# Kernel tuning notes

Measured on AMD Instinct MI355X. Metric: run time of the kernel, lower is better.

## Reference

```python
import jax, jax.numpy as jnp
import numpy as np

N, F_NODE, F_FLOW, H, E, B, L = 131072, 64, 16, 128, 2097152, 256, 32


def setup_inputs() -> dict:
    key = jax.random.key(0)
    ks = jax.random.split(key, 24)
    gn = lambda k, s, sc: jax.random.normal(k, s, jnp.float32) * sc
    s_in = 1.0 / np.sqrt(F_NODE)
    s_h = 1.0 / np.sqrt(H)
    s_f = 1.0 / np.sqrt(F_FLOW)
    s_c = 1.0 / np.sqrt(2 * H + H // 2)
    inp = {
        "x": gn(ks[0], (N, F_NODE), 1.0),
        "edge_index": jax.random.randint(ks[1], (2, E), 0, N),
        "batch": jnp.sort(jax.random.randint(ks[2], (N,), 0, B)),
        "path_idx": jax.random.randint(ks[3], (B, L), 0, N),
        "path_len": jax.random.randint(ks[4], (B,), 1, L + 1),
        "flow": gn(ks[5], (B, F_FLOW), 1.0),
        # SAGEConv1: out = mean_agg(x_j) @ Wl.T + b + x_i @ Wr.T
        "Wl1": gn(ks[6], (H, F_NODE), s_in), "Wr1": gn(ks[7], (H, F_NODE), s_in), "b1": gn(ks[8], (H,), s_in),
        "Wl2": gn(ks[9], (H, H), s_h), "Wr2": gn(ks[10], (H, H), s_h), "b2": gn(ks[11], (H,), s_h),
        # LSTM (torch gate order i,f,g,o)
        "Wih": gn(ks[12], (4 * H, H), s_h), "Whh": gn(ks[13], (4 * H, H), s_h),
        "bih": gn(ks[14], (4 * H,), s_h), "bhh": gn(ks[15], (4 * H,), s_h),
        # flow encoder Linear(F_FLOW, H//2)
        "Wf": gn(ks[16], (H // 2, F_FLOW), s_f), "bf": gn(ks[17], (H // 2,), s_f),
        # scorer MLP: Linear(2H+H//2, H) -> ReLU -> Linear(H, 1)
        "Ws1": gn(ks[18], (H, 2 * H + H // 2), s_c), "bs1": gn(ks[19], (H,), s_c),
        "Ws2": gn(ks[20], (1, H), s_h), "bs2": gn(ks[21], (1,), s_h),
    }
    return inp


def _sage(x, src, dst, Wl, Wr, b, n):
    agg = jax.ops.segment_sum(x[src], dst, num_segments=n)  # [n, d]
    cnt = jax.ops.segment_sum(jnp.ones((src.shape[0],), x.dtype), dst, num_segments=n)
    mean = agg / jnp.maximum(cnt, 1.0)[:, None]
    return mean @ Wl.T + b + x @ Wr.T


def _lstm_final_h(seq, valid, Wih, Whh, bih, bhh):
    # seq: [B, L, H], valid: [B, L] bool; returns h at each path's last valid step
    b, l, h = seq.shape
    h0 = jnp.zeros((b, h), seq.dtype)

    def step(carry, inp):
        hp, cp = carry
        x_t, v = inp  # [B,H], [B]
        gates = x_t @ Wih.T + hp @ Whh.T + bih + bhh
        i, f, g, o = jnp.split(gates, 4, axis=-1)
        c_new = jax.nn.sigmoid(f) * cp + jax.nn.sigmoid(i) * jnp.tanh(g)
        h_new = jax.nn.sigmoid(o) * jnp.tanh(c_new)
        m = v[:, None]
        return (jnp.where(m, h_new, hp), jnp.where(m, c_new, cp)), None

    (hf, _), _ = jax.lax.scan(step, (h0, h0),
                              (jnp.swapaxes(seq, 0, 1), jnp.swapaxes(valid, 0, 1)))
    return hf


def reference(x, edge_index, batch, path_idx, path_len, flow,
              Wl1, Wr1, b1, Wl2, Wr2, b2,
              Wih, Whh, bih, bhh, Wf, bf, Ws1, bs1, Ws2, bs2):
    n = x.shape[0]
    src, dst = edge_index[0], edge_index[1]
    h1 = jax.nn.relu(_sage(x, src, dst, Wl1, Wr1, b1, n))
    node_emb = jax.nn.relu(_sage(h1, src, dst, Wl2, Wr2, b2, n))

    # global mean pool per graph
    gsum = jax.ops.segment_sum(node_emb, batch, num_segments=B)
    gcnt = jax.ops.segment_sum(jnp.ones((n,), node_emb.dtype), batch, num_segments=B)
    graph_emb = gsum / jnp.maximum(gcnt, 1.0)[:, None]  # [B, H]

    flow_emb = jax.nn.relu(flow @ Wf.T + bf)  # [B, H//2]

    path_seq = node_emb[path_idx]  # [B, L, H]
    valid = jnp.arange(L)[None, :] < path_len[:, None]  # [B, L]
    path_emb = _lstm_final_h(path_seq, valid, Wih, Whh, bih, bhh)  # [B, H]

    combined = jnp.concatenate([graph_emb, path_emb, flow_emb], axis=-1)
    hidden = jax.nn.relu(combined @ Ws1.T + bs1)
    scores = hidden @ Ws2.T + bs2  # [B, 1]
    return scores[:, 0]  # matches torch.cat of per-path [1] outputs -> [B]
```

## Files before the change

### kernel.cpp

```cpp
#include <hip/hip_runtime.h>
#include <hip/hip_bf16.h>

#define N_NODES 131072
#define N_EDGES 2097152
#define BATCHES 256
#define LPATH   32
#define NB   256
#define NPB  512
#define GB   256
#define EPB  8192
#define EBL_CAP 9216

typedef __hip_bfloat16 bf16;
using short8  = __attribute__((ext_vector_type(8))) short;
using floatx4 = __attribute__((ext_vector_type(4))) float;
using floatx2 = __attribute__((ext_vector_type(2))) float;

__device__ __forceinline__ float bl(unsigned u){ union {unsigned x; float f;} c; c.x = u << 16; return c.f; }
__device__ __forceinline__ float bh(unsigned u){ union {unsigned x; float f;} c; c.x = u & 0xffff0000u; return c.f; }
__device__ __forceinline__ unsigned packbf(float lo, float hi){
  bf16 l = __float2bfloat16(lo), h = __float2bfloat16(hi);
  unsigned short lu, hu;
  __builtin_memcpy(&lu, &l, 2); __builtin_memcpy(&hu, &h, 2);
  return (unsigned)lu | ((unsigned)hu << 16);
}
__device__ __forceinline__ float frcp(float x){ return __builtin_amdgcn_rcpf(x); }
__device__ __forceinline__ float sigf(float x){ return frcp(1.f + __expf(-x)); }
__device__ __forceinline__ float tanh_fast(float x){ return fmaf(2.f, frcp(1.f + __expf(-2.f * x)), -1.f); }

__global__ void mega0_k(const float* __restrict__ x, unsigned* __restrict__ xb8, bf16* __restrict__ Acat1,
                        const int* __restrict__ dst, int* __restrict__ cntA,
                        const float* __restrict__ Wl1, const float* __restrict__ Wr1,
                        const float* __restrict__ Wl2, const float* __restrict__ Wr2,
                        const float* __restrict__ Wih, const float* __restrict__ Whh,
                        const float* __restrict__ bih, const float* __restrict__ bhh,
                        bf16* __restrict__ Wcat1, bf16* __restrict__ Wcat2,
                        bf16* __restrict__ WihB, bf16* __restrict__ WhhB, float* __restrict__ bsumF,
                        const int* __restrict__ batch, int* __restrict__ starts){
  __shared__ int h[NB];
  int bid = blockIdx.x, tid = threadIdx.x;
  if (bid < 8192){
    int g = bid * 256 + tid;
    int n = g >> 4, p = g & 15;
    float4 v = *(const float4*)(x + (size_t)n * 64 + p * 4);
    uint2 wb; wb.x = packbf(v.x, v.y); wb.y = packbf(v.z, v.w);
    *(uint2*)(Acat1 + (size_t)n * 128 + 64 + p * 4) = wb;
    int w = 0;
    w = __builtin_amdgcn_cvt_pk_fp8_f32(v.x, v.y, w, false);
    w = __builtin_amdgcn_cvt_pk_fp8_f32(v.z, v.w, w, true);
    xb8[(size_t)n * 16 + p] = (unsigned)w;
  } else if (bid < 8448){
    int cb = bid - 8192;
    h[tid] = 0;
    __syncthreads();
    int base = cb * EPB;
    #pragma unroll
    for (int i = 0; i < EPB / 256; ++i){
      int d = dst[base + i * 256 + tid];
      atomicAdd(&h[d >> 9], 1);
    }
    __syncthreads();
    cntA[tid * GB + cb] = h[tid];
  } else if (bid < 9155){
    int g = (bid - 8448) * 256 + tid;
    if (g < 16384) {
      int hh = g >> 7, k = g & 127;
      float v = (k < 64) ? Wl1[hh * 64 + k] : Wr1[hh * 64 + (k - 64)];
      Wcat1[g] = __float2bfloat16(v);
    } else if (g < 49152) {
      int q = g - 16384;
      int hh = q >> 8, k = q & 255;
      float v = (k < 128) ? Wl2[hh * 128 + k] : Wr2[hh * 128 + (k - 128)];
      Wcat2[q] = __float2bfloat16(v);
    } else if (g < 114688) {
      int q = g - 49152;
      WihB[q] = __float2bfloat16(Wih[q]);
    } else if (g < 180224) {
      int q = g - 114688;
      WhhB[q] = __float2bfloat16(Whh[q]);
    } else if (g < 180736) {
      int k = g - 180224;
      bsumF[k] = bih[k] + bhh[k];
    }
  } else {
    int b = tid;
    int lo = 0, hi = N_NODES;
    while (lo < hi){ int mid = (lo + hi) >> 1; if (batch[mid] < b) lo = mid + 1; else hi = mid; }
    starts[b] = lo;
    if (b == 0) starts[BATCHES] = N_NODES;
  }
}

__global__ void scan1_k(const int* __restrict__ cnt, int* __restrict__ ofsA, int* __restrict__ bsum){
  __shared__ int sh[256];
  int t = threadIdx.x, i = blockIdx.x * 256 + t;
  int v = cnt[i];
  sh[t] = v; __syncthreads();
  int inc = v;
  for (int d = 1; d < 256; d <<= 1){
    int add = (t >= d) ? sh[t - d] : 0;
    __syncthreads();
    inc += add; sh[t] = inc;
    __syncthreads();
  }
  ofsA[i] = inc - v;
  if (t == 255) bsum[blockIdx.x] = inc;
}

__global__ void passA2_k(const int* __restrict__ src, const int* __restrict__ dst,
                         const int* __restrict__ ofsA, const int* __restrict__ bsum,
                         unsigned* __restrict__ ebuf){
  __shared__ int cur[NB];
  __shared__ int sc[NB];
  int tid = threadIdx.x;
  int v = bsum[tid];
  sc[tid] = v; __syncthreads();
  int inc = v;
  for (int d = 1; d < NB; d <<= 1){
    int add = (tid >= d) ? sc[tid - d] : 0;
    __syncthreads();
    inc += add; sc[tid] = inc;
    __syncthreads();
  }
  cur[tid] = ofsA[tid * GB + blockIdx.x] + (inc - v);
  __syncthreads();
  int base = blockIdx.x * EPB;
  #pragma unroll
  for (int i = 0; i < EPB / 256; ++i){
    int e = base + i * 256 + tid;
    int s = src[e], d = dst[e];
    int p = atomicAdd(&cur[d >> 9], 1);
    ebuf[p] = (unsigned)s | ((unsigned)(d & (NPB - 1)) << 17);
  }
}

__global__ void passB_k(const unsigned* __restrict__ ebuf, const int* __restrict__ bsum,
                        int* __restrict__ offs, int* __restrict__ srcS){
  __shared__ unsigned ebl[EBL_CAP];
  __shared__ int ncnt[NPB];
  __shared__ int pairs[256];
  __shared__ int nofs[NPB];
  __shared__ int sc[NB];
  int k = blockIdx.x, tid = threadIdx.x;
  int v = bsum[tid];
  sc[tid] = v; __syncthreads();
  int inc0 = v;
  for (int d = 1; d < NB; d <<= 1){
    int add = (tid >= d) ? sc[tid - d] : 0;
    __syncthreads();
    inc0 += add; sc[tid] = inc0;
    __syncthreads();
  }
  sc[tid] = inc0 - v;
  __syncthreads();
  int bs = sc[k];
  int be = (k < NB - 1) ? sc[k + 1] : N_EDGES;
  int cnt = be - bs;
  int stg = cnt < EBL_CAP ? cnt : EBL_CAP;
  for (int i = tid; i < stg; i += 256) ebl[i] = ebuf[bs + i];
  ncnt[tid] = 0; ncnt[tid + 256] = 0;
  __syncthreads();
  for (int i = tid; i < cnt; i += 256){
    unsigned w = (i < stg) ? ebl[i] : ebuf[bs + i];
    atomicAdd(&ncnt[w >> 17], 1);
  }
  __syncthreads();
  int p = ncnt[2 * tid] + ncnt[2 * tid + 1];
  pairs[tid] = p;
  __syncthreads();
  int inc = p;
  for (int d = 1; d < 256; d <<= 1){
    int add = (tid >= d) ? pairs[tid - d] : 0;
    __syncthreads();
    inc += add; pairs[tid] = inc;
    __syncthreads();
  }
  int ex = inc - p;
  nofs[2 * tid]     = ex;
  nofs[2 * tid + 1] = ex + ncnt[2 * tid];
  __syncthreads();
  offs[k * NPB + tid]       = bs + nofs[tid];
  offs[k * NPB + tid + 256] = bs + nofs[tid + 256];
  if (k == NB - 1 && tid == 0) offs[N_NODES] = N_EDGES;
  ncnt[tid] = nofs[tid]; ncnt[tid + 256] = nofs[tid + 256];
  __syncthreads();
  for (int i = tid; i < cnt; i += 256){
    unsigned w = (i < stg) ? ebl[i] : ebuf[bs + i];
    int loc = w >> 17, sv = w & 0x1FFFF;
    int pp = atomicAdd(&ncnt[loc], 1);
    srcS[bs + pp] = sv;
  }
}

__global__ void agg1_k(const unsigned* __restrict__ xb8, const int* __restrict__ offs,
                       const int* __restrict__ srcS, bf16* __restrict__ Acat1){
  int wid = threadIdx.x >> 6, lane = threadIdx.x & 63;
  int q = lane >> 4;
  int slot = (lane >> 3) & 1, fl = lane & 7;
  int n = blockIdx.x * 16 + wid * 4 + q;
  int s = offs[n], e = offs[n + 1];
  floatx2 a0={0,0}, a1={0,0}, a2={0,0}, a3={0,0};
  floatx2 c0={0,0}, c1={0,0}, c2={0,0}, c3={0,0};
  int i = s + slot;
  for (; i + 6 < e; i += 8){
    int sv0 = srcS[i], sv1 = srcS[i + 2], sv2 = srcS[i + 4], sv3 = srcS[i + 6];
    uint2 u = *(const uint2*)(xb8 + (size_t)sv0 * 16 + fl * 2);
    uint2 v = *(const uint2*)(xb8 + (size_t)sv1 * 16 + fl * 2);
    uint2 w = *(const uint2*)(xb8 + (size_t)sv2 * 16 + fl * 2);
    uint2 z = *(const uint2*)(xb8 + (size_t)sv3 * 16 + fl * 2);
    a0 += __builtin_amdgcn_cvt_pk_f32_fp8(u.x, false);
    a1 += __builtin_amdgcn_cvt_pk_f32_fp8(u.x, true);
    a2 += __builtin_amdgcn_cvt_pk_f32_fp8(u.y, false);
    a3 += __builtin_amdgcn_cvt_pk_f32_fp8(u.y, true);
    c0 += __builtin_amdgcn_cvt_pk_f32_fp8(v.x, false);
    c1 += __builtin_amdgcn_cvt_pk_f32_fp8(v.x, true);
    c2 += __builtin_amdgcn_cvt_pk_f32_fp8(v.y, false);
    c3 += __builtin_amdgcn_cvt_pk_f32_fp8(v.y, true);
    a0 += __builtin_amdgcn_cvt_pk_f32_fp8(w.x, false);
    a1 += __builtin_amdgcn_cvt_pk_f32_fp8(w.x, true);
    a2 += __builtin_amdgcn_cvt_pk_f32_fp8(w.y, false);
    a3 += __builtin_amdgcn_cvt_pk_f32_fp8(w.y, true);
    c0 += __builtin_amdgcn_cvt_pk_f32_fp8(z.x, false);
    c1 += __builtin_amdgcn_cvt_pk_f32_fp8(z.x, true);
    c2 += __builtin_amdgcn_cvt_pk_f32_fp8(z.y, false);
    c3 += __builtin_amdgcn_cvt_pk_f32_fp8(z.y, true);
  }
  for (; i < e; i += 2){
    int sv0 = srcS[i];
    uint2 u = *(const uint2*)(xb8 + (size_t)sv0 * 16 + fl * 2);
    a0 += __builtin_amdgcn_cvt_pk_f32_fp8(u.x, false);
    a1 += __builtin_amdgcn_cvt_pk_f32_fp8(u.x, true);
    a2 += __builtin_amdgcn_cvt_pk_f32_fp8(u.y, false);
    a3 += __builtin_amdgcn_cvt_pk_f32_fp8(u.y, true);
  }
  a0 += c0; a1 += c1; a2 += c2; a3 += c3;
  float f[8] = {a0.x, a0.y, a1.x, a1.y, a2.x, a2.y, a3.x, a3.y};
  #pragma unroll
  for (int j = 0; j < 8; ++j)
    f[j] += __shfl_xor(f[j], 8);
  if (slot == 0){
    int d = e - s; if (d < 1) d = 1;
    float inv = 1.f / (float)d;
    uint4 w;
    w.x = packbf(f[0] * inv, f[1] * inv);
    w.y = packbf(f[2] * inv, f[3] * inv);
    w.z = packbf(f[4] * inv, f[5] * inv);
    w.w = packbf(f[6] * inv, f[7] * inv);
    *(uint4*)(Acat1 + (size_t)n * 128 + fl * 8) = w;
  }
}

__global__ __launch_bounds__(256) void gemmf8_k(const bf16* __restrict__ A, const bf16* __restrict__ W,
                                                const float* __restrict__ bias,
                                                bf16* __restrict__ h1B, unsigned* __restrict__ h1f8){
  __shared__ bf16 Wl[128][136];
  __shared__ unsigned char f8t[64][144];
  int tid = threadIdx.x;
  int wid = tid >> 6, lane = tid & 63;
  int l16 = lane & 15, quad = lane >> 4;
  int rowBase = blockIdx.x * 64 + wid * 16;
  floatx4 acc[8] = {};
  for (int c = tid; c < 2048; c += 256){
    int r = c >> 4, kc = (c & 15) << 3;
    *(uint4*)(&Wl[r][kc]) = *(const uint4*)(W + (size_t)r * 128 + kc);
  }
  __syncthreads();
  for (int kk = 0; kk < 4; ++kk){
    short8 af = *(const short8*)(A + (size_t)(rowBase + l16) * 128 + kk * 32 + quad * 8);
    #pragma unroll
    for (int c = 0; c < 8; ++c){
      short8 bq = *(const short8*)(&Wl[c * 16 + l16][kk * 32 + quad * 8]);
      acc[c] = __builtin_amdgcn_mfma_f32_16x16x32_bf16(af, bq, acc[c], 0, 0, 0);
    }
  }
  #pragma unroll
  for (int c = 0; c < 8; ++c){
    int col = c * 16 + l16;
    float bv = bias[col];
    #pragma unroll
    for (int r = 0; r < 4; ++r){
      int rl = wid * 16 + quad * 4 + r;
      float v = fmaxf(acc[c][r] + bv, 0.f);
      h1B[(size_t)(blockIdx.x * 64 + rl) * 128 + col] = __float2bfloat16(v);
      unsigned pk = (unsigned)__builtin_amdgcn_cvt_pk_fp8_f32(v, v, 0, false);
      f8t[rl][col] = (unsigned char)(pk & 0xFF);
    }
  }
  __syncthreads();
  for (int it = tid; it < 512; it += 256){
    int row = it >> 3, seg = it & 7;
    uint4 val = *(const uint4*)(&f8t[row][seg * 16]);
    *(uint4*)((char*)h1f8 + (size_t)(blockIdx.x * 64 + row) * 128 + seg * 16) = val;
  }
}

__global__ void agg2_k(const int* __restrict__ offs, const int* __restrict__ srcS,
                       const unsigned* __restrict__ h1f8, bf16* __restrict__ meanB){
  int wid = threadIdx.x >> 6, lane = threadIdx.x & 63;
  int half = lane >> 5;
  int slot = (lane >> 4) & 1, fl = lane & 15;
  int n = blockIdx.x * 8 + wid * 2 + half;
  int s = offs[n], e = offs[n + 1];
  floatx2 a0={0,0}, a1={0,0}, a2={0,0}, a3={0,0};
  floatx2 c0={0,0}, c1={0,0}, c2={0,0}, c3={0,0};
  int i = s + slot;
  for (; i + 6 < e; i += 8){
    int sv0 = srcS[i], sv1 = srcS[i + 2], sv2 = srcS[i + 4], sv3 = srcS[i + 6];
    uint2 u = *(const uint2*)(h1f8 + (size_t)sv0 * 32 + fl * 2);
    uint2 v = *(const uint2*)(h1f8 + (size_t)sv1 * 32 + fl * 2);
    uint2 w = *(const uint2*)(h1f8 + (size_t)sv2 * 32 + fl * 2);
    uint2 z = *(const uint2*)(h1f8 + (size_t)sv3 * 32 + fl * 2);
    a0 += __builtin_amdgcn_cvt_pk_f32_fp8(u.x, false);
    a1 += __builtin_amdgcn_cvt_pk_f32_fp8(u.x, true);
    a2 += __builtin_amdgcn_cvt_pk_f32_fp8(u.y, false);
    a3 += __builtin_amdgcn_cvt_pk_f32_fp8(u.y, true);
    c0 += __builtin_amdgcn_cvt_pk_f32_fp8(v.x, false);
    c1 += __builtin_amdgcn_cvt_pk_f32_fp8(v.x, true);
    c2 += __builtin_amdgcn_cvt_pk_f32_fp8(v.y, false);
    c3 += __builtin_amdgcn_cvt_pk_f32_fp8(v.y, true);
    a0 += __builtin_amdgcn_cvt_pk_f32_fp8(w.x, false);
    a1 += __builtin_amdgcn_cvt_pk_f32_fp8(w.x, true);
    a2 += __builtin_amdgcn_cvt_pk_f32_fp8(w.y, false);
    a3 += __builtin_amdgcn_cvt_pk_f32_fp8(w.y, true);
    c0 += __builtin_amdgcn_cvt_pk_f32_fp8(z.x, false);
    c1 += __builtin_amdgcn_cvt_pk_f32_fp8(z.x, true);
    c2 += __builtin_amdgcn_cvt_pk_f32_fp8(z.y, false);
    c3 += __builtin_amdgcn_cvt_pk_f32_fp8(z.y, true);
  }
  for (; i < e; i += 2){
    int sv0 = srcS[i];
    uint2 u = *(const uint2*)(h1f8 + (size_t)sv0 * 32 + fl * 2);
    a0 += __builtin_amdgcn_cvt_pk_f32_fp8(u.x, false);
    a1 += __builtin_amdgcn_cvt_pk_f32_fp8(u.x, true);
    a2 += __builtin_amdgcn_cvt_pk_f32_fp8(u.y, false);
    a3 += __builtin_amdgcn_cvt_pk_f32_fp8(u.y, true);
  }
  a0 += c0; a1 += c1; a2 += c2; a3 += c3;
  float f[8] = {a0.x, a0.y, a1.x, a1.y, a2.x, a2.y, a3.x, a3.y};
  #pragma unroll
  for (int j = 0; j < 8; ++j)
    f[j] += __shfl_xor(f[j], 16);
  if (slot == 0){
    int d = e - s; if (d < 1) d = 1;
    float inv = 1.f / (float)d;
    uint4 w;
    w.x = packbf(f[0] * inv, f[1] * inv);
    w.y = packbf(f[2] * inv, f[3] * inv);
    w.z = packbf(f[4] * inv, f[5] * inv);
    w.w = packbf(f[6] * inv, f[7] * inv);
    *(uint4*)(meanB + (size_t)n * 128 + fl * 8) = w;
  }
}

__global__ __launch_bounds__(256) void gemm2sp_k(const bf16* __restrict__ A0, const bf16* __restrict__ A1,
                                                 const bf16* __restrict__ W, const float* __restrict__ bias,
                                                 bf16* __restrict__ out){
  __shared__ bf16 Wl[128][136];
  int tid = threadIdx.x;
  int wid = tid >> 6, lane = tid & 63;
  int l16 = lane & 15, quad = lane >> 4;
  int rowBase = blockIdx.x * 64 + wid * 16;
  floatx4 acc[8] = {};
  #pragma unroll
  for (int ks = 0; ks < 2; ++ks){
    __syncthreads();
    for (int c = tid; c < 2048; c += 256){
      int r = c >> 4, kc = (c & 15) << 3;
      *(uint4*)(&Wl[r][kc]) = *(const uint4*)(W + (size_t)r * 256 + ks * 128 + kc);
    }
    __syncthreads();
    const bf16* Ab = ks ? A1 : A0;
    for (int kk = 0; kk < 4; ++kk){
      short8 af = *(const short8*)(Ab + (size_t)(rowBase + l16) * 128 + kk * 32 + quad * 8);
      #pragma unroll
      for (int c = 0; c < 8; ++c){
        short8 bq = *(const short8*)(&Wl[c * 16 + l16][kk * 32 + quad * 8]);
        acc[c] = __builtin_amdgcn_mfma_f32_16x16x32_bf16(af, bq, acc[c], 0, 0, 0);
      }
    }
  }
  #pragma unroll
  for (int c = 0; c < 8; ++c){
    int col = c * 16 + l16;
    float bv = bias[col];
    #pragma unroll
    for (int r = 0; r < 4; ++r){
      int row = rowBase + quad * 4 + r;
      out[(size_t)row * 128 + col] = __float2bfloat16(fmaxf(acc[c][r] + bv, 0.f));
    }
  }
}

__global__ __launch_bounds__(256) void tail0_k(const bf16* __restrict__ ne, const bf16* __restrict__ W,
                                               const float* __restrict__ bias, float* __restrict__ pre,
                                               const int* __restrict__ ridx,
                                               const int* __restrict__ starts,
                                               const float* __restrict__ flow, const float* __restrict__ Wf,
                                               const float* __restrict__ bfv, float* __restrict__ comb){
  __shared__ bf16 Wl[128][136];
  __shared__ float sh[4][128];
  int bid = blockIdx.x, tid = threadIdx.x;
  if (bid < 512){
    int bx = bid >> 2, by = bid & 3;
    int wid = tid >> 6, lane = tid & 63;
    int l16 = lane & 15, quad = lane >> 4;
    int rowBase = bx * 64 + wid * 16;
    int colGroup = by * 128;
    int arow = ridx[rowBase + l16];
    floatx4 acc[8] = {};
    for (int c = tid; c < 2048; c += 256){
      int r = c >> 4, kc = (c & 15) << 3;
      *(uint4*)(&Wl[r][kc]) = *(const uint4*)(W + (size_t)(colGroup + r) * 128 + kc);
    }
    __syncthreads();
    for (int kk = 0; kk < 4; ++kk){
      short8 af = *(const short8*)(ne + (size_t)arow * 128 + kk * 32 + quad * 8);
      #pragma unroll
      for (int c = 0; c < 8; ++c){
        short8 bq = *(const short8*)(&Wl[c * 16 + l16][kk * 32 + quad * 8]);
        acc[c] = __builtin_amdgcn_mfma_f32_16x16x32_bf16(af, bq, acc[c], 0, 0, 0);
      }
    }
    #pragma unroll
    for (int c = 0; c < 8; ++c){
      int col = colGroup + c * 16 + l16;
      float bv = bias[col];
      #pragma unroll
      for (int r = 0; r < 4; ++r){
        int row = rowBase + quad * 4 + r;
        pre[(size_t)row * 512 + col] = acc[c][r] + bv;
      }
    }
  } else if (bid < 768){
    int b = bid - 512;
    int q = tid >> 6, lane = tid & 63;
    int s = starts[b], e = starts[b + 1];
    float a0 = 0.f, a1 = 0.f;
    for (int i = s + q; i < e; i += 4){
      unsigned u = *(const unsigned*)(ne + (size_t)i * 128 + lane * 2);
      a0 += bl(u); a1 += bh(u);
    }
    sh[q][lane * 2] = a0; sh[q][lane * 2 + 1] = a1;
    __syncthreads();
    if (tid < 128){
      int f = tid;
      float tot = sh[0][f] + sh[1][f] + sh[2][f] + sh[3][f];
      int d = e - s; if (d < 1) d = 1;
      comb[b * 320 + f] = tot / (float)d;
    }
  } else {
    int g = (bid - 768) * 256 + tid;
    int b = g >> 6, j = g & 63;
    float acc = bfv[j];
    for (int k = 0; k < 16; ++k)
      acc += flow[b * 16 + k] * Wf[j * 16 + k];
    comb[b * 320 + 256 + j] = fmaxf(acc, 0.f);
  }
}

__global__ __launch_bounds__(256, 1) void lstm_k(const bf16* __restrict__ Whh, const float* __restrict__ pre,
                                                 const int* __restrict__ path_len, float* __restrict__ comb){
  __shared__ bf16 hbuf[2][16][136];
  int tid = threadIdx.x;
  int w = tid >> 6, lane = tid & 63;
  int l16 = lane & 15, quad = lane >> 4;
  int b0 = blockIdx.x * 16;

  short8 wb[4][2][4];
  #pragma unroll
  for (int q = 0; q < 4; ++q)
    #pragma unroll
    for (int hf = 0; hf < 2; ++hf){
      const bf16* rp = Whh + (size_t)(q * 128 + w * 32 + hf * 16 + l16) * 128 + quad * 8;
      #pragma unroll
      for (int ks = 0; ks < 4; ++ks) wb[q][hf][ks] = *(const short8*)(rp + ks * 32);
    }

  int lenr[4];
  #pragma unroll
  for (int r = 0; r < 4; ++r){
    int L = path_len[b0 + quad * 4 + r];
    if (L < 1) L = 1; if (L > LPATH) L = LPATH;
    lenr[r] = L;
  }
  int maxlen = 1;
  for (int i = 0; i < 16; ++i){
    int L = path_len[b0 + i];
    if (L > LPATH) L = LPATH;
    if (L > maxlen) maxlen = L;
  }

  for (int i = tid; i < 1088; i += 256) ((unsigned*)&hbuf[0][0][0])[i] = 0;

  const float* pb[4];
  #pragma unroll
  for (int r = 0; r < 4; ++r)
    pb[r] = pre + (size_t)(b0 + quad * 4 + r) * LPATH * 512 + w * 32 + l16;

  float pv[4][2][4];
  #pragma unroll
  for (int q = 0; q < 4; ++q)
    #pragma unroll
    for (int hf = 0; hf < 2; ++hf)
      #pragma unroll
      for (int r = 0; r < 4; ++r)
        pv[q][hf][r] = pb[r][q * 128 + hf * 16];

  float cst[2][4] = {}, hst[2][4] = {};

  for (int t = 0; t < maxlen; ++t){
    int cur = t & 1, nxt = cur ^ 1;
    __syncthreads();
    short8 af[4];
    #pragma unroll
    for (int ks = 0; ks < 4; ++ks)
      af[ks] = *(const short8*)(&hbuf[cur][l16][ks * 32 + quad * 8]);
    int tn = (t + 1 < maxlen) ? t + 1 : t;
    float pnext[4][2][4];
    #pragma unroll
    for (int q = 0; q < 4; ++q)
      #pragma unroll
      for (int hf = 0; hf < 2; ++hf)
        #pragma unroll
        for (int r = 0; r < 4; ++r)
          pnext[q][hf][r] = pb[r][tn * 512 + q * 128 + hf * 16];
    floatx4 acc[4][2];
    #pragma unroll
    for (int q = 0; q < 4; ++q)
      #pragma unroll
      for (int hf = 0; hf < 2; ++hf){
        acc[q][hf][0] = pv[q][hf][0]; acc[q][hf][1] = pv[q][hf][1];
        acc[q][hf][2] = pv[q][hf][2]; acc[q][hf][3] = pv[q][hf][3];
      }
    #pragma unroll
    for (int ks = 0; ks < 4; ++ks)
      #pragma unroll
      for (int q = 0; q < 4; ++q)
        #pragma unroll
        for (int hf = 0; hf < 2; ++hf)
          acc[q][hf] = __builtin_amdgcn_mfma_f32_16x16x32_bf16(af[ks], wb[q][hf][ks], acc[q][hf], 0, 0, 0);
    #pragma unroll
    for (int hf = 0; hf < 2; ++hf)
      #pragma unroll
      for (int r = 0; r < 4; ++r){
        float ig = sigf(acc[0][hf][r]);
        float fg = sigf(acc[1][hf][r]);
        float gg = tanh_fast(acc[2][hf][r]);
        float og = sigf(acc[3][hf][r]);
        float cn = fmaf(fg, cst[hf][r], ig * gg);
        float hn = og * tanh_fast(cn);
        bool vld = t < lenr[r];
        cst[hf][r] = vld ? cn : cst[hf][r];
        hst[hf][r] = vld ? hn : hst[hf][r];
        hbuf[nxt][quad * 4 + r][w * 32 + hf * 16 + l16] = __float2bfloat16(hst[hf][r]);
      }
    #pragma unroll
    for (int q = 0; q < 4; ++q)
      #pragma unroll
      for (int hf = 0; hf < 2; ++hf)
        #pragma unroll
        for (int r = 0; r < 4; ++r)
          pv[q][hf][r] = pnext[q][hf][r];
  }

  #pragma unroll
  for (int hf = 0; hf < 2; ++hf)
    #pragma unroll
    for (int r = 0; r < 4; ++r)
      comb[(b0 + quad * 4 + r) * 320 + 128 + w * 32 + hf * 16 + l16] = hst[hf][r];
}

__global__ void head_k(const float* __restrict__ comb, const float* __restrict__ Ws1, const float* __restrict__ bs1,
                       const float* __restrict__ Ws2, const float* __restrict__ bs2, float* __restrict__ out){
  __shared__ float cl[320];
  __shared__ float red[128];
  int b = blockIdx.x, j = threadIdx.x;
  for (int k = j; k < 320; k += 128) cl[k] = comb[b * 320 + k];
  __syncthreads();
  float acc = bs1[j];
  const float4* wr = (const float4*)(Ws1 + (size_t)j * 320);
  #pragma unroll 4
  for (int kc = 0; kc < 80; ++kc){
    float4 u = wr[kc];
    int k = kc * 4;
    acc += u.x * cl[k] + u.y * cl[k + 1] + u.z * cl[k + 2] + u.w * cl[k + 3];
  }
  float hv = fmaxf(acc, 0.f);
  red[j] = hv * Ws2[j];
  __syncthreads();
  for (int s = 64; s > 0; s >>= 1){ if (j < s) red[j] += red[j + s]; __syncthreads(); }
  if (j == 0) out[b] = red[0] + bs2[0];
}

constexpr size_t OFF_OFFS   = 0;
constexpr size_t OFF_CNTA   = 524544;
constexpr size_t OFF_OFSA   = OFF_CNTA   + 262144;
constexpr size_t OFF_BSUM   = OFF_OFSA   + 262144;
constexpr size_t OFF_STARTS = OFF_BSUM   + 1024;
constexpr size_t OFF_SRCS   = OFF_STARTS + 2048;
constexpr size_t OFF_WCAT1  = OFF_SRCS   + 8388608;
constexpr size_t OFF_WCAT2  = OFF_WCAT1  + 32768;
constexpr size_t OFF_WIHB   = OFF_WCAT2  + 65536;
constexpr size_t OFF_WHHB   = OFF_WIHB   + 131072;
constexpr size_t OFF_BSUMF  = OFF_WHHB   + 131072;
constexpr size_t OFF_COMB   = OFF_BSUMF  + 2048;
constexpr size_t OFF_R1     = OFF_COMB   + 327680;
constexpr size_t OFF_R2     = OFF_R1     + 33554432;
constexpr size_t OFF_EBUF   = OFF_R2;
constexpr size_t OFF_H1B    = OFF_R2;
constexpr size_t OFF_PRE    = OFF_R2;
constexpr size_t OFF_XB8    = OFF_R2 + 33554432;
constexpr size_t OFF_H1F8   = OFF_R2 + 33554432;
constexpr size_t OFF_NE     = OFF_R2 + 33554432;

extern "C" void kernel_launch(void* const* d_in, const int* in_sizes, int n_in,
                              void* d_out, int out_size, void* d_ws, size_t ws_size,
                              hipStream_t stream){
  const float* x      = (const float*)d_in[0];
  const int* edge     = (const int*)d_in[1];
  const int* batch    = (const int*)d_in[2];
  const int* path_idx = (const int*)d_in[3];
  const int* path_len = (const int*)d_in[4];
  const float* flow   = (const float*)d_in[5];
  const float* Wl1 = (const float*)d_in[6];
  const float* Wr1 = (const float*)d_in[7];
  const float* b1  = (const float*)d_in[8];
  const float* Wl2 = (const float*)d_in[9];
  const float* Wr2 = (const float*)d_in[10];
  const float* b2  = (const float*)d_in[11];
  const float* Wih = (const float*)d_in[12];
  const float* Whh = (const float*)d_in[13];
  const float* bih = (const float*)d_in[14];
  const float* bhh = (const float*)d_in[15];
  const float* Wf  = (const float*)d_in[16];
  const float* bfv = (const float*)d_in[17];
  const float* Ws1 = (const float*)d_in[18];
  const float* bs1 = (const float*)d_in[19];
  const float* Ws2 = (const float*)d_in[20];
  const float* bs2 = (const float*)d_in[21];

  char* ws = (char*)d_ws;
  int* offs    = (int*)(ws + OFF_OFFS);
  int* cntA    = (int*)(ws + OFF_CNTA);
  int* ofsA    = (int*)(ws + OFF_OFSA);
  int* bsum    = (int*)(ws + OFF_BSUM);
  int* starts  = (int*)(ws + OFF_STARTS);
  int* srcS    = (int*)(ws + OFF_SRCS);
  bf16* Wcat1  = (bf16*)(ws + OFF_WCAT1);
  bf16* Wcat2  = (bf16*)(ws + OFF_WCAT2);
  bf16* WihB   = (bf16*)(ws + OFF_WIHB);
  bf16* WhhB   = (bf16*)(ws + OFF_WHHB);
  float* bsumF = (float*)(ws + OFF_BSUMF);
  float* comb  = (float*)(ws + OFF_COMB);
  bf16* Acat1  = (bf16*)(ws + OFF_R1);
  bf16* meanB  = (bf16*)(ws + OFF_R1);
  unsigned* ebuf = (unsigned*)(ws + OFF_EBUF);
  bf16* h1B    = (bf16*)(ws + OFF_H1B);
  float* pre   = (float*)(ws + OFF_PRE);
  unsigned* xb8  = (unsigned*)(ws + OFF_XB8);
  unsigned* h1f8 = (unsigned*)(ws + OFF_H1F8);
  bf16* node_emb = (bf16*)(ws + OFF_NE);

  mega0_k<<<9156, 256, 0, stream>>>(x, xb8, Acat1, edge + N_EDGES, cntA,
                                    Wl1, Wr1, Wl2, Wr2, Wih, Whh, bih, bhh,
                                    Wcat1, Wcat2, WihB, WhhB, bsumF, batch, starts);
  scan1_k<<<NB, 256, 0, stream>>>(cntA, ofsA, bsum);
  passA2_k<<<GB, 256, 0, stream>>>(edge, edge + N_EDGES, ofsA, bsum, ebuf);
  passB_k<<<NB, 256, 0, stream>>>(ebuf, bsum, offs, srcS);
  agg1_k<<<N_NODES / 16, 256, 0, stream>>>(xb8, offs, srcS, Acat1);
  gemmf8_k<<<N_NODES / 64, 256, 0, stream>>>(Acat1, Wcat1, b1, h1B, h1f8);
  agg2_k<<<N_NODES / 8, 256, 0, stream>>>(offs, srcS, h1f8, meanB);
  gemm2sp_k<<<N_NODES / 64, 256, 0, stream>>>(meanB, h1B, Wcat2, b2, node_emb);
  tail0_k<<<832, 256, 0, stream>>>(node_emb, WihB, bsumF, pre, path_idx, starts, flow, Wf, bfv, comb);
  lstm_k<<<BATCHES / 16, 256, 0, stream>>>(WhhB, pre, path_len, comb);
  head_k<<<BATCHES, 128, 0, stream>>>(comb, Ws1, bs1, Ws2, bs2, (float*)d_out);
}
```

Baseline: 389.1 us.

## Fuse graph mean-pool into GEMM epilogue and drop separate scan kernel

Removes the scan1 kernel by having passA2 and passB each recompute per-bucket totals and prefixes directly from the count matrix. Also moves the global mean-pool sum into the second SAGE GEMM epilogue: each block segment-reduces its rows by batch id in shared memory and atomically adds into comb, with the divide by node count deferred to the head kernel. The aim is fewer launches and no second read of node_emb, at the cost of redundant 256-element row sums per thread, more shared memory in the GEMM, and float atomics whose order is nondeterministic.

```diff
diff --git a/kernel.cpp b/kernel.cpp
--- a/kernel.cpp
+++ b/kernel.cpp
@@ -36,7 +36,7 @@
                         const float* __restrict__ bih, const float* __restrict__ bhh,
                         bf16* __restrict__ Wcat1, bf16* __restrict__ Wcat2,
                         bf16* __restrict__ WihB, bf16* __restrict__ WhhB, float* __restrict__ bsumF,
-                        const int* __restrict__ batch, int* __restrict__ starts){
+                        const int* __restrict__ batch, int* __restrict__ starts, float* __restrict__ comb){
   __shared__ int h[NB];
   int bid = blockIdx.x, tid = threadIdx.x;
   if (bid < 8192){
@@ -82,49 +82,42 @@
       int k = g - 180224;
       bsumF[k] = bih[k] + bhh[k];
     }
-  } else {
+  } else if (bid == 9155){
     int b = tid;
     int lo = 0, hi = N_NODES;
     while (lo < hi){ int mid = (lo + hi) >> 1; if (batch[mid] < b) lo = mid + 1; else hi = mid; }
     starts[b] = lo;
     if (b == 0) starts[BATCHES] = N_NODES;
-  }
-}
-
-__global__ void scan1_k(const int* __restrict__ cnt, int* __restrict__ ofsA, int* __restrict__ bsum){
-  __shared__ int sh[256];
-  int t = threadIdx.x, i = blockIdx.x * 256 + t;
-  int v = cnt[i];
-  sh[t] = v; __syncthreads();
-  int inc = v;
-  for (int d = 1; d < 256; d <<= 1){
-    int add = (t >= d) ? sh[t - d] : 0;
-    __syncthreads();
-    inc += add; sh[t] = inc;
-    __syncthreads();
-  }
-  ofsA[i] = inc - v;
-  if (t == 255) bsum[blockIdx.x] = inc;
+  } else {
+    int g = (bid - 9156) * 256 + tid;
+    int b = g >> 7, f = g & 127;
+    comb[b * 320 + f] = 0.f;
+  }
 }
 
 __global__ void passA2_k(const int* __restrict__ src, const int* __restrict__ dst,
-                         const int* __restrict__ ofsA, const int* __restrict__ bsum,
-                         unsigned* __restrict__ ebuf){
+                         const int* __restrict__ cntA, unsigned* __restrict__ ebuf){
   __shared__ int cur[NB];
   __shared__ int sc[NB];
-  int tid = threadIdx.x;
-  int v = bsum[tid];
-  sc[tid] = v; __syncthreads();
-  int inc = v;
+  int tid = threadIdx.x, bid = blockIdx.x;
+  const int* row = cntA + tid * GB;
+  int pref = 0, tot = 0;
+  for (int j = 0; j < GB; ++j){
+    int c = row[j];
+    tot += c;
+    if (j < bid) pref += c;
+  }
+  sc[tid] = tot; __syncthreads();
+  int inc = tot;
   for (int d = 1; d < NB; d <<= 1){
     int add = (tid >= d) ? sc[tid - d] : 0;
     __syncthreads();
     inc += add; sc[tid] = inc;
     __syncthreads();
   }
-  cur[tid] = ofsA[tid * GB + blockIdx.x] + (inc - v);
-  __syncthreads();
-  int base = blockIdx.x * EPB;
+  cur[tid] = (inc - tot) + pref;
+  __syncthreads();
+  int base = bid * EPB;
   #pragma unroll
   for (int i = 0; i < EPB / 256; ++i){
     int e = base + i * 256 + tid;
@@ -134,7 +127,7 @@
   }
 }
 
-__global__ void passB_k(const unsigned* __restrict__ ebuf, const int* __restrict__ bsum,
+__global__ void passB_k(const unsigned* __restrict__ ebuf, const int* __restrict__ cntA,
                         int* __restrict__ offs, int* __restrict__ srcS){
   __shared__ unsigned ebl[EBL_CAP];
   __shared__ int ncnt[NPB];
@@ -142,16 +135,18 @@
   __shared__ int nofs[NPB];
   __shared__ int sc[NB];
   int k = blockIdx.x, tid = threadIdx.x;
-  int v = bsum[tid];
-  sc[tid] = v; __syncthreads();
-  int inc0 = v;
+  const int* row = cntA + tid * GB;
+  int tot = 0;
+  for (int j = 0; j < GB; ++j) tot += row[j];
+  sc[tid] = tot; __syncthreads();
+  int inc0 = tot;
   for (int d = 1; d < NB; d <<= 1){
     int add = (tid >= d) ? sc[tid - d] : 0;
     __syncthreads();
     inc0 += add; sc[tid] = inc0;
     __syncthreads();
   }
-  sc[tid] = inc0 - v;
+  sc[tid] = inc0 - tot;
   __syncthreads();
   int bs = sc[k];
   int be = (k < NB - 1) ? sc[k + 1] : N_EDGES;
@@ -354,8 +349,11 @@
 
 __global__ __launch_bounds__(256) void gemm2sp_k(const bf16* __restrict__ A0, const bf16* __restrict__ A1,
                                                  const bf16* __restrict__ W, const float* __restrict__ bias,
-                                                 bf16* __restrict__ out){
+                                                 bf16* __restrict__ out,
+                                                 const int* __restrict__ batch, float* __restrict__ comb){
   __shared__ bf16 Wl[128][136];
+  __shared__ float vals[64][132];
+  __shared__ int bid64[64];
   int tid = threadIdx.x;
   int wid = tid >> 6, lane = tid & 63;
   int l16 = lane & 15, quad = lane >> 4;
@@ -379,26 +377,39 @@
       }
     }
   }
+  if (tid < 64) bid64[tid] = batch[blockIdx.x * 64 + tid];
   #pragma unroll
   for (int c = 0; c < 8; ++c){
     int col = c * 16 + l16;
     float bv = bias[col];
     #pragma unroll
     for (int r = 0; r < 4; ++r){
-      int row = rowBase + quad * 4 + r;
-      out[(size_t)row * 128 + col] = __float2bfloat16(fmaxf(acc[c][r] + bv, 0.f));
-    }
-  }
+      int rl = wid * 16 + quad * 4 + r;
+      float v = fmaxf(acc[c][r] + bv, 0.f);
+      out[(size_t)(blockIdx.x * 64 + rl) * 128 + col] = __float2bfloat16(v);
+      vals[rl][col] = v;
+    }
+  }
+  __syncthreads();
+  int col = tid & 127, hf = tid >> 7;
+  int r0 = hf * 32;
+  int curb = bid64[r0];
+  float run = 0.f;
+  #pragma unroll 8
+  for (int r = r0; r < r0 + 32; ++r){
+    int bb = bid64[r];
+    if (bb != curb){ atomicAdd(&comb[curb * 320 + col], run); run = 0.f; curb = bb; }
+    run += vals[r][col];
+  }
+  atomicAdd(&comb[curb * 320 + col], run);
 }
 
 __global__ __launch_bounds__(256) void tail0_k(const bf16* __restrict__ ne, const bf16* __restrict__ W,
                                                const float* __restrict__ bias, float* __restrict__ pre,
                                                const int* __restrict__ ridx,
-                                               const int* __restrict__ starts,
                                                const float* __restrict__ flow, const float* __restrict__ Wf,
                                                const float* __restrict__ bfv, float* __restrict__ comb){
   __shared__ bf16 Wl[128][136];
-  __shared__ float sh[4][128];
   int bid = blockIdx.x, tid = threadIdx.x;
   if (bid < 512){
     int bx = bid >> 2, by = bid & 3;
@@ -431,25 +442,8 @@
         pre[(size_t)row * 512 + col] = acc[c][r] + bv;
       }
     }
-  } else if (bid < 768){
-    int b = bid - 512;
-    int q = tid >> 6, lane = tid & 63;
-    int s = starts[b], e = starts[b + 1];
-    float a0 = 0.f, a1 = 0.f;
-    for (int i = s + q; i < e; i += 4){
-      unsigned u = *(const unsigned*)(ne + (size_t)i * 128 + lane * 2);
-      a0 += bl(u); a1 += bh(u);
-    }
-    sh[q][lane * 2] = a0; sh[q][lane * 2 + 1] = a1;
-    __syncthreads();
-    if (tid < 128){
-      int f = tid;
-      float tot = sh[0][f] + sh[1][f] + sh[2][f] + sh[3][f];
-      int d = e - s; if (d < 1) d = 1;
-      comb[b * 320 + f] = tot / (float)d;
-    }
   } else {
-    int g = (bid - 768) * 256 + tid;
+    int g = (bid - 512) * 256 + tid;
     int b = g >> 6, j = g & 63;
     float acc = bfv[j];
     for (int k = 0; k < 16; ++k)
@@ -570,12 +564,18 @@
       comb[(b0 + quad * 4 + r) * 320 + 128 + w * 32 + hf * 16 + l16] = hst[hf][r];
 }
 
-__global__ void head_k(const float* __restrict__ comb, const float* __restrict__ Ws1, const float* __restrict__ bs1,
+__global__ void head_k(const float* __restrict__ comb, const int* __restrict__ starts,
+                       const float* __restrict__ Ws1, const float* __restrict__ bs1,
                        const float* __restrict__ Ws2, const float* __restrict__ bs2, float* __restrict__ out){
   __shared__ float cl[320];
   __shared__ float red[128];
   int b = blockIdx.x, j = threadIdx.x;
-  for (int k = j; k < 320; k += 128) cl[k] = comb[b * 320 + k];
+  int d = starts[b + 1] - starts[b]; if (d < 1) d = 1;
+  float invd = 1.f / (float)d;
+  for (int k = j; k < 320; k += 128){
+    float v = comb[b * 320 + k];
+    cl[k] = (k < 128) ? v * invd : v;
+  }
   __syncthreads();
   float acc = bs1[j];
   const float4* wr = (const float4*)(Ws1 + (size_t)j * 320);
@@ -594,9 +594,7 @@
 
 constexpr size_t OFF_OFFS   = 0;
 constexpr size_t OFF_CNTA   = 524544;
-constexpr size_t OFF_OFSA   = OFF_CNTA   + 262144;
-constexpr size_t OFF_BSUM   = OFF_OFSA   + 262144;
-constexpr size_t OFF_STARTS = OFF_BSUM   + 1024;
+constexpr size_t OFF_STARTS = OFF_CNTA   + 262144;
 constexpr size_t OFF_SRCS   = OFF_STARTS + 2048;
 constexpr size_t OFF_WCAT1  = OFF_SRCS   + 8388608;
 constexpr size_t OFF_WCAT2  = OFF_WCAT1  + 32768;
@@ -642,8 +640,6 @@
   char* ws = (char*)d_ws;
   int* offs    = (int*)(ws + OFF_OFFS);
   int* cntA    = (int*)(ws + OFF_CNTA);
-  int* ofsA    = (int*)(ws + OFF_OFSA);
-  int* bsum    = (int*)(ws + OFF_BSUM);
   int* starts  = (int*)(ws + OFF_STARTS);
   int* srcS    = (int*)(ws + OFF_SRCS);
   bf16* Wcat1  = (bf16*)(ws + OFF_WCAT1);
@@ -661,17 +657,16 @@
   unsigned* h1f8 = (unsigned*)(ws + OFF_H1F8);
   bf16* node_emb = (bf16*)(ws + OFF_NE);
 
-  mega0_k<<<9156, 256, 0, stream>>>(x, xb8, Acat1, edge + N_EDGES, cntA,
+  mega0_k<<<9284, 256, 0, stream>>>(x, xb8, Acat1, edge + N_EDGES, cntA,
                                     Wl1, Wr1, Wl2, Wr2, Wih, Whh, bih, bhh,
-                                    Wcat1, Wcat2, WihB, WhhB, bsumF, batch, starts);
-  scan1_k<<<NB, 256, 0, stream>>>(cntA, ofsA, bsum);
-  passA2_k<<<GB, 256, 0, stream>>>(edge, edge + N_EDGES, ofsA, bsum, ebuf);
-  passB_k<<<NB, 256, 0, stream>>>(ebuf, bsum, offs, srcS);
+                                    Wcat1, Wcat2, WihB, WhhB, bsumF, batch, starts, comb);
+  passA2_k<<<GB, 256, 0, stream>>>(edge, edge + N_EDGES, cntA, ebuf);
+  passB_k<<<NB, 256, 0, stream>>>(ebuf, cntA, offs, srcS);
   agg1_k<<<N_NODES / 16, 256, 0, stream>>>(xb8, offs, srcS, Acat1);
   gemmf8_k<<<N_NODES / 64, 256, 0, stream>>>(Acat1, Wcat1, b1, h1B, h1f8);
   agg2_k<<<N_NODES / 8, 256, 0, stream>>>(offs, srcS, h1f8, meanB);
-  gemm2sp_k<<<N_NODES / 64, 256, 0, stream>>>(meanB, h1B, Wcat2, b2, node_emb);
-  tail0_k<<<832, 256, 0, stream>>>(node_emb, WihB, bsumF, pre, path_idx, starts, flow, Wf, bfv, comb);
+  gemm2sp_k<<<N_NODES / 64, 256, 0, stream>>>(meanB, h1B, Wcat2, b2, node_emb, batch, comb);
+  tail0_k<<<576, 256, 0, stream>>>(node_emb, WihB, bsumF, pre, path_idx, flow, Wf, bfv, comb);
   lstm_k<<<BATCHES / 16, 256, 0, stream>>>(WhhB, pre, path_len, comb);
-  head_k<<<BATCHES, 128, 0, stream>>>(comb, Ws1, bs1, Ws2, bs2, (float*)d_out);
-}
+  head_k<<<BATCHES, 128, 0, stream>>>(comb, starts, Ws1, bs1, Ws2, bs2, (float*)d_out);
+}
```

After: 389.4 us. Within noise of the previous version (+0.1%).
